# Optimization experiments

Measured on AMD Instinct MI355X. Metric: run time of the kernel, lower is better.

The kernel has to match this reference:

```python
import jax, jax.numpy as jnp
import numpy as np

N_NODES = 50000
N_EDGES = 800000
F_IN = 64
HID = 64
N_GRAPHS = 256
BN_EPS = 1e-5


def setup_inputs() -> dict:
    key = jax.random.key(0)
    ks = jax.random.split(key, 16)
    inp = {
        'x': jax.random.normal(ks[0], (N_NODES, F_IN), dtype=jnp.float32),
        'edge_index': jax.random.randint(ks[1], (2, N_EDGES), 0, N_NODES, dtype=jnp.int64),
        'edge_weight': jax.random.uniform(ks[2], (N_EDGES,), dtype=jnp.float32),
        'batch': jnp.sort(jax.random.randint(ks[3], (N_NODES,), 0, N_GRAPHS, dtype=jnp.int64)),
    }
    def lin(k, fi, fo):
        s = 1.0 / np.sqrt(fi)
        kw, kb = jax.random.split(k)
        return (jax.random.uniform(kw, (fi, fo), jnp.float32, -s, s),
                jax.random.uniform(kb, (fo,), jnp.float32, -s, s))
    inp['W1'], inp['b1'] = lin(ks[4], F_IN, HID)
    inp['W2'], inp['b2'] = lin(ks[5], HID, HID)
    inp['W3'], inp['b3'] = lin(ks[6], HID, HID)
    inp['fcW1'], inp['fcb1'] = lin(ks[7], HID, HID)
    inp['fcW2'], inp['fcb2'] = lin(ks[8], HID, 1)
    for i, k in zip((1, 2, 3), ks[9:12]):
        inp[f'g{i}'] = jnp.ones((HID,), jnp.float32)
        inp[f'be{i}'] = jnp.zeros((HID,), jnp.float32)
    return inp


def gin_conv(x, src, dst, edge_weight, W, b):
    # weighted scatter-add aggregation: agg[dst] += w_e * x[src]
    msg = x[src] * edge_weight[:, None]            # [E, d]
    agg = jax.ops.segment_sum(msg, dst, num_segments=x.shape[0])  # [N, d]
    return (x + agg) @ W + b                       # GIN eps=0, nn = Linear


def batch_norm(x, gamma, beta):
    mu = jnp.mean(x, axis=0)
    var = jnp.var(x, axis=0)
    return (x - mu) * jax.lax.rsqrt(var + BN_EPS) * gamma + beta


def reference(x, edge_index, edge_weight, batch,
              W1, b1, W2, b2, W3, b3, fcW1, fcb1, fcW2, fcb2,
              g1, be1, g2, be2, g3, be3):
    src, dst = edge_index[0], edge_index[1]
    h = batch_norm(jax.nn.relu(gin_conv(x, src, dst, edge_weight, W1, b1)), g1, be1)
    h = batch_norm(jax.nn.relu(gin_conv(h, src, dst, edge_weight, W2, b2)), g2, be2)
    h = batch_norm(gin_conv(h, src, dst, edge_weight, W3, b3), g3, be3)
    pooled = jax.ops.segment_sum(h, batch, num_segments=N_GRAPHS)  # global_add_pool
    h = jax.nn.relu(pooled)
    h = jax.nn.relu(h @ fcW1 + fcb1)
    # dropout is identity in eval / deterministic reference
    return (h @ fcW2 + fcb2).reshape(-1)
```

## Files before the change

kernel.cpp:

```cpp
#include <hip/hip_runtime.h>
#include <hip/hip_bf16.h>


#define NN 50000
#define NE 800000
#define FD 64
#define NG 256
#define CAP 64
#define NBKT 16
#define BN_EPS 1e-5f

#define NPART 8
#define PSIZE 6250
#define ECHUNK 2048
#define NCHUNK ((NE + ECHUNK - 1) / ECHUNK)
#define NBUILD (NCHUNK * NPART)
#define NCVT   ((NN * 16) / 256)

__device__ __forceinline__ float4 dec4(uint2 a) {
    float4 f;
    f.x = __uint_as_float(a.x << 16);
    f.y = __uint_as_float(a.x & 0xFFFF0000u);
    f.z = __uint_as_float(a.y << 16);
    f.w = __uint_as_float(a.y & 0xFFFF0000u);
    return f;
}
__device__ __forceinline__ unsigned rbf(float f) {
    unsigned u = __float_as_uint(f);
    return (u + 0x7FFFu + ((u >> 16) & 1u)) >> 16;
}
__device__ __forceinline__ uint2 enc4(float4 v) {
    uint2 o;
    o.x = rbf(v.x) | (rbf(v.y) << 16);
    o.y = rbf(v.z) | (rbf(v.w) << 16);
    return o;
}

__global__ __launch_bounds__(256) void build_cvt_kernel(
    const int* __restrict__ src, const int* __restrict__ dst,
    const float* __restrict__ ew, int* __restrict__ cursor,
    unsigned* __restrict__ slots,
    const float4* __restrict__ xin, uint2* __restrict__ xout)
{
    int bid = blockIdx.x;
    int tid = threadIdx.x;
    if (bid < NBUILD) {
        int part  = bid & 7;
        int chunk = bid >> 3;
        int base  = chunk * ECHUNK;
        #pragma unroll
        for (int i = 0; i < ECHUNK; i += 256) {
            int e = base + i + tid;
            if (e < NE) {
                int d = dst[e];
                if (d / PSIZE == part) {
                    int pos = atomicAdd(&cursor[d], 1) & (CAP - 1);
                    slots[(size_t)d * CAP + pos] =
                        ((unsigned)src[e] << 16) | rbf(ew[e]);
                }
            }
        }
    } else {
        int i = (bid - NBUILD) * 256 + tid;
        xout[i] = enc4(xin[i]);
    }
}

__global__ __launch_bounds__(256) void agg_layer_kernel(
    const uint2* __restrict__ h, const int* __restrict__ deg,
    const unsigned* __restrict__ slots,
    const float* __restrict__ prev_buckets,
    const float* __restrict__ prev_gamma, const float* __restrict__ prev_beta,
    const float* __restrict__ W, const float* __restrict__ b,
    uint2* __restrict__ y, float* __restrict__ buckets, int relu_flag,
    const int* __restrict__ batch, float* __restrict__ pooled)
{
    __shared__ float Ws[FD * FD];
    __shared__ float ps1[4][FD];
    __shared__ float ps2[4][FD];
    __shared__ float afs[FD], cfs[FD];
    int tid  = threadIdx.x;
    int wave = tid >> 6, lane = tid & 63;
    int g = lane >> 4, l = lane & 15;
    int node = blockIdx.x * 4 + wave;

    {
        float4* Wv = (float4*)Ws;
        const float4* Wg = (const float4*)W;
        #pragma unroll
        for (int i = 0; i < 4; i++) Wv[tid + 256 * i] = Wg[tid + 256 * i];
    }

    unsigned ms = slots[(size_t)node * CAP + lane];
    int dg = deg[node];
    float4 self = dec4(h[(size_t)node * 16 + l]);
    if (dg > CAP) dg = CAP;

    if (prev_buckets) {
        int f = tid & 63, q = tid >> 6;
        float S1 = 0.f, S2 = 0.f;
        #pragma unroll
        for (int i = 0; i < 4; i++) {
            int bkt = q * 4 + i;
            S1 += prev_buckets[bkt * 128 + f];
            S2 += prev_buckets[bkt * 128 + FD + f];
        }
        ps1[q][f] = S1;
        ps2[q][f] = S2;
    }
    __syncthreads();
    if (prev_buckets && tid < FD) {
        float s1 = ps1[0][tid] + ps1[1][tid] + ps1[2][tid] + ps1[3][tid];
        float s2 = ps2[0][tid] + ps2[1][tid] + ps2[2][tid] + ps2[3][tid];
        float mu  = s1 * (1.f / NN);
        float var = s2 * (1.f / NN) - mu * mu;
        float a = prev_gamma[tid] * rsqrtf(var + BN_EPS);
        afs[tid] = a;
        cfs[tid] = prev_beta[tid] - mu * a;
    }
    __syncthreads();

    float4 af = make_float4(1.f, 1.f, 1.f, 1.f);
    float4 cf = make_float4(0.f, 0.f, 0.f, 0.f);
    if (prev_buckets) {
        af = ((const float4*)afs)[l];
        cf = ((const float4*)cfs)[l];
    }

    float4 acc = make_float4(0.f, 0.f, 0.f, 0.f);
    float wsum = 0.f;
    int nIter = (dg + 15) >> 4;
    for (int i = 0; i < nIter; i++) {
        unsigned m[4]; uint2 r[4];
        #pragma unroll
        for (int j = 0; j < 4; j++)
            m[j] = (unsigned)__shfl((int)ms, 16 * i + 4 * j + g, 64);
        #pragma unroll
        for (int j = 0; j < 4; j++)
            r[j] = h[(size_t)(m[j] >> 16) * 16 + l];
        #pragma unroll
        for (int j = 0; j < 4; j++) {
            float w = __uint_as_float(m[j] << 16);
            float4 v = dec4(r[j]);
            wsum += w;
            acc.x = fmaf(w, v.x, acc.x); acc.y = fmaf(w, v.y, acc.y);
            acc.z = fmaf(w, v.z, acc.z); acc.w = fmaf(w, v.w, acc.w);
        }
    }
    acc.x += __shfl_xor(acc.x, 16, 64); acc.y += __shfl_xor(acc.y, 16, 64);
    acc.z += __shfl_xor(acc.z, 16, 64); acc.w += __shfl_xor(acc.w, 16, 64);
    wsum  += __shfl_xor(wsum, 16, 64);
    acc.x += __shfl_xor(acc.x, 32, 64); acc.y += __shfl_xor(acc.y, 32, 64);
    acc.z += __shfl_xor(acc.z, 32, 64); acc.w += __shfl_xor(acc.w, 32, 64);
    wsum  += __shfl_xor(wsum, 32, 64);

    float4 raw;
    raw.x = self.x + acc.x; raw.y = self.y + acc.y;
    raw.z = self.z + acc.z; raw.w = self.w + acc.w;

    float sw = 1.0f + wsum;
    float4 hin;
    hin.x = fmaf(af.x, raw.x, cf.x * sw);
    hin.y = fmaf(af.y, raw.y, cf.y * sw);
    hin.z = fmaf(af.z, raw.z, cf.z * sw);
    hin.w = fmaf(af.w, raw.w, cf.w * sw);

    const float4* __restrict__ WsV = (const float4*)Ws;
    float4 yp = make_float4(0.f, 0.f, 0.f, 0.f);
    #pragma unroll
    for (int kk = 0; kk < 4; kk++) {
        int srcl = 4 * g + kk;
        float a0 = __shfl(hin.x, srcl, 64);
        float a1 = __shfl(hin.y, srcl, 64);
        float a2 = __shfl(hin.z, srcl, 64);
        float a3 = __shfl(hin.w, srcl, 64);
        int k0 = 16 * g + 4 * kk;
        float4 w0 = WsV[(k0 + 0) * 16 + l];
        float4 w1 = WsV[(k0 + 1) * 16 + l];
        float4 w2 = WsV[(k0 + 2) * 16 + l];
        float4 w3 = WsV[(k0 + 3) * 16 + l];
        yp.x = fmaf(a0, w0.x, yp.x); yp.y = fmaf(a0, w0.y, yp.y);
        yp.z = fmaf(a0, w0.z, yp.z); yp.w = fmaf(a0, w0.w, yp.w);
        yp.x = fmaf(a1, w1.x, yp.x); yp.y = fmaf(a1, w1.y, yp.y);
        yp.z = fmaf(a1, w1.z, yp.z); yp.w = fmaf(a1, w1.w, yp.w);
        yp.x = fmaf(a2, w2.x, yp.x); yp.y = fmaf(a2, w2.y, yp.y);
        yp.z = fmaf(a2, w2.z, yp.z); yp.w = fmaf(a2, w2.w, yp.w);
        yp.x = fmaf(a3, w3.x, yp.x); yp.y = fmaf(a3, w3.y, yp.y);
        yp.z = fmaf(a3, w3.z, yp.z); yp.w = fmaf(a3, w3.w, yp.w);
    }
    yp.x += __shfl_xor(yp.x, 16, 64); yp.y += __shfl_xor(yp.y, 16, 64);
    yp.z += __shfl_xor(yp.z, 16, 64); yp.w += __shfl_xor(yp.w, 16, 64);
    yp.x += __shfl_xor(yp.x, 32, 64); yp.y += __shfl_xor(yp.y, 32, 64);
    yp.z += __shfl_xor(yp.z, 32, 64); yp.w += __shfl_xor(yp.w, 32, 64);

    float4 bias = ((const float4*)b)[l];
    float4 yv;
    yv.x = yp.x + bias.x; yv.y = yp.y + bias.y;
    yv.z = yp.z + bias.z; yv.w = yp.w + bias.w;
    if (relu_flag) {
        yv.x = fmaxf(yv.x, 0.f); yv.y = fmaxf(yv.y, 0.f);
        yv.z = fmaxf(yv.z, 0.f); yv.w = fmaxf(yv.w, 0.f);
    }
    if (g == 0) {
        if (!pooled)
            y[(size_t)node * 16 + l] = enc4(yv);
        ((float4*)&ps1[wave][0])[l] = yv;
        float4 sq;
        sq.x = yv.x * yv.x; sq.y = yv.y * yv.y;
        sq.z = yv.z * yv.z; sq.w = yv.w * yv.w;
        ((float4*)&ps2[wave][0])[l] = sq;
    }
    __syncthreads();
    if (tid < FD) {
        float a = ps1[0][tid] + ps1[1][tid] + ps1[2][tid] + ps1[3][tid];
        float q = ps2[0][tid] + ps2[1][tid] + ps2[2][tid] + ps2[3][tid];
        float* bk = buckets + (blockIdx.x & (NBKT - 1)) * 128;
        atomicAdd(&bk[tid], a);
        atomicAdd(&bk[FD + tid], q);
        if (pooled) {
            int n0 = blockIdx.x * 4;
            int b0 = batch[n0], b3 = batch[n0 + 3];
            if (b0 == b3) {
                atomicAdd(&pooled[b0 * FD + tid], a);
            } else {
                #pragma unroll
                for (int w = 0; w < 4; w++)
                    atomicAdd(&pooled[batch[n0 + w] * FD + tid],
                              ps1[w][tid]);
            }
        }
    }
}

__global__ __launch_bounds__(256) void head_kernel(
    const float* __restrict__ pooled, const int* __restrict__ batch,
    const float* __restrict__ buckets3,
    const float* __restrict__ g3, const float* __restrict__ be3,
    const float* __restrict__ fcW1, const float* __restrict__ fcb1,
    const float* __restrict__ fcW2, const float* __restrict__ fcb2,
    float* __restrict__ out)
{
    __shared__ float red[8][FD];
    __shared__ int bounds[2];
    int tid = threadIdx.x;
    int g = blockIdx.x;

    {
        int f = tid & 63, q = tid >> 6;
        float S1 = 0.f, S2 = 0.f;
        #pragma unroll
        for (int i = 0; i < 4; i++) {
            int bkt = q * 4 + i;
            S1 += buckets3[bkt * 128 + f];
            S2 += buckets3[bkt * 128 + FD + f];
        }
        red[q][f]     = S1;
        red[4 + q][f] = S2;
    }
    if (tid < 2) {
        int target = g + tid;
        int lo = 0, hi = NN;
        while (lo < hi) {
            int mid = (lo + hi) >> 1;
            if (batch[mid] < target) lo = mid + 1; else hi = mid;
        }
        bounds[tid] = lo;
    }
    __syncthreads();

    if (tid < 64) {
        float s1 = red[0][tid] + red[1][tid] + red[2][tid] + red[3][tid];
        float s2 = red[4][tid] + red[5][tid] + red[6][tid] + red[7][tid];
        float mu  = s1 * (1.f / NN);
        float var = s2 * (1.f / NN) - mu * mu;
        float a = g3[tid] * rsqrtf(var + BN_EPS);
        float c = be3[tid] - mu * a;

        float cnt = (float)(bounds[1] - bounds[0]);
        float p = pooled[g * FD + tid];
        p = fmaf(a, p, c * cnt);
        p = fmaxf(p, 0.f);
        float acc1 = fcb1[tid];
        #pragma unroll
        for (int k = 0; k < FD; k++) {
            float pk = __shfl(p, k, 64);
            acc1 = fmaf(pk, fcW1[k * FD + tid], acc1);
        }
        acc1 = fmaxf(acc1, 0.f);
        float prod = acc1 * fcW2[tid];
        #pragma unroll
        for (int off = 32; off > 0; off >>= 1)
            prod += __shfl_xor(prod, off, 64);
        if (tid == 0) out[g] = prod + fcb2[0];
    }
}

extern "C" void kernel_launch(void* const* d_in, const int* in_sizes, int n_in,
                              void* d_out, int out_size, void* d_ws, size_t ws_size,
                              hipStream_t stream) {
    const float* x     = (const float*)d_in[0];
    const int*   ei    = (const int*)d_in[1];
    const float* ew    = (const float*)d_in[2];
    const int*   batch = (const int*)d_in[3];
    const float* W1 = (const float*)d_in[4],  *b1 = (const float*)d_in[5];
    const float* W2 = (const float*)d_in[6],  *b2 = (const float*)d_in[7];
    const float* W3 = (const float*)d_in[8],  *b3 = (const float*)d_in[9];
    const float* fcW1 = (const float*)d_in[10], *fcb1 = (const float*)d_in[11];
    const float* fcW2 = (const float*)d_in[12], *fcb2 = (const float*)d_in[13];
    const float* g1 = (const float*)d_in[14], *be1 = (const float*)d_in[15];
    const float* g2 = (const float*)d_in[16], *be2 = (const float*)d_in[17];
    const float* g3 = (const float*)d_in[18], *be3 = (const float*)d_in[19];
    float* out = (float*)d_out;

    const int* srcp = ei;
    const int* dstp = ei + NE;

    char* ws = (char*)d_ws;
    size_t off = 0;
    auto take = [&](size_t bytes) -> char* {
        char* p = ws + off;
        off += (bytes + 255) & ~(size_t)255;
        return p;
    };
    uint2*    xbf   = (uint2*)   take((size_t)NN * FD * 2);
    uint2*    bufA  = (uint2*)   take((size_t)NN * FD * 2);
    uint2*    bufB  = (uint2*)   take((size_t)NN * FD * 2);
    size_t zero_base = off;
    unsigned* slots = (unsigned*)take((size_t)NN * CAP * 4);
    int*      cursor= (int*)     take((size_t)NN * 4);
    float*    buckets=(float*)   take((size_t)3 * NBKT * 128 * 4);
    float*    pooled =(float*)   take((size_t)NG * FD * 4);
    size_t zero_bytes = off - zero_base;
    (void)ws_size; (void)n_in; (void)in_sizes; (void)out_size;

    hipMemsetAsync(ws + zero_base, 0, zero_bytes, stream);

    build_cvt_kernel<<<NBUILD + NCVT, 256, 0, stream>>>(srcp, dstp, ew,
                                                        cursor, slots,
                                                        (const float4*)x, xbf);

    const int gridA = NN / 4;

    float* bk1 = buckets + 0 * NBKT * 128;
    float* bk2 = buckets + 1 * NBKT * 128;
    float* bk3 = buckets + 2 * NBKT * 128;

    agg_layer_kernel<<<gridA, 256, 0, stream>>>(xbf, cursor, slots,
                                                nullptr, nullptr, nullptr,
                                                W1, b1, bufA, bk1, 1,
                                                nullptr, nullptr);
    agg_layer_kernel<<<gridA, 256, 0, stream>>>(bufA, cursor, slots,
                                                bk1, g1, be1,
                                                W2, b2, bufB, bk2, 1,
                                                nullptr, nullptr);
    agg_layer_kernel<<<gridA, 256, 0, stream>>>(bufB, cursor, slots,
                                                bk2, g2, be2,
                                                W3, b3, bufA, bk3, 0,
                                                batch, pooled);
    head_kernel<<<NG, 256, 0, stream>>>(pooled, batch, bk3, g3, be3,
                                        fcW1, fcb1, fcW2, fcb2, out);
}
```

Measured before the change: 261.3 us.

## Hoist BN affine into tiny kernel, template layer modes, defer W smem store

The per-block reduction of the previous layer's BN statistics buckets, along with its two block barriers, moves out of the 12500-block aggregation kernel into a single 64-thread kernel that writes the scale and shift vectors. The aggregation kernel becomes a template on layer mode, so the relu, output-store and pooling branches resolve at compile time. The weight matrix is now loaded into registers at kernel start and only written to shared memory after the gather loop, so the global load overlaps the gather and one barrier remains. In exchange it adds two extra kernel launches and holds more registers across the gather loop, which may lower occupancy.

```diff
diff --git a/kernel.cpp b/kernel.cpp
--- a/kernel.cpp
+++ b/kernel.cpp
@@ -66,65 +66,57 @@
     }
 }
 
+__global__ __launch_bounds__(64) void bn_affine_kernel(
+    const float* __restrict__ bk,
+    const float* __restrict__ gamma, const float* __restrict__ beta,
+    float* __restrict__ afc)
+{
+    int t = threadIdx.x;
+    float S1 = 0.f, S2 = 0.f;
+    #pragma unroll
+    for (int i = 0; i < NBKT; i++) {
+        S1 += bk[i * 128 + t];
+        S2 += bk[i * 128 + FD + t];
+    }
+    float mu  = S1 * (1.f / NN);
+    float var = S2 * (1.f / NN) - mu * mu;
+    float a = gamma[t] * rsqrtf(var + BN_EPS);
+    afc[t]      = a;
+    afc[FD + t] = beta[t] - mu * a;
+}
+
+template<int MODE>
 __global__ __launch_bounds__(256) void agg_layer_kernel(
     const uint2* __restrict__ h, const int* __restrict__ deg,
     const unsigned* __restrict__ slots,
-    const float* __restrict__ prev_buckets,
-    const float* __restrict__ prev_gamma, const float* __restrict__ prev_beta,
+    const float* __restrict__ afc,
     const float* __restrict__ W, const float* __restrict__ b,
-    uint2* __restrict__ y, float* __restrict__ buckets, int relu_flag,
+    uint2* __restrict__ y, float* __restrict__ buckets,
     const int* __restrict__ batch, float* __restrict__ pooled)
 {
     __shared__ float Ws[FD * FD];
     __shared__ float ps1[4][FD];
     __shared__ float ps2[4][FD];
-    __shared__ float afs[FD], cfs[FD];
     int tid  = threadIdx.x;
     int wave = tid >> 6, lane = tid & 63;
     int g = lane >> 4, l = lane & 15;
     int node = blockIdx.x * 4 + wave;
 
-    {
-        float4* Wv = (float4*)Ws;
-        const float4* Wg = (const float4*)W;
-        #pragma unroll
-        for (int i = 0; i < 4; i++) Wv[tid + 256 * i] = Wg[tid + 256 * i];
-    }
+    const float4* __restrict__ Wg = (const float4*)W;
+    float4 wr0 = Wg[tid];
+    float4 wr1 = Wg[tid + 256];
+    float4 wr2 = Wg[tid + 512];
+    float4 wr3 = Wg[tid + 768];
 
     unsigned ms = slots[(size_t)node * CAP + lane];
     int dg = deg[node];
     float4 self = dec4(h[(size_t)node * 16 + l]);
     if (dg > CAP) dg = CAP;
 
-    if (prev_buckets) {
-        int f = tid & 63, q = tid >> 6;
-        float S1 = 0.f, S2 = 0.f;
-        #pragma unroll
-        for (int i = 0; i < 4; i++) {
-            int bkt = q * 4 + i;
-            S1 += prev_buckets[bkt * 128 + f];
-            S2 += prev_buckets[bkt * 128 + FD + f];
-        }
-        ps1[q][f] = S1;
-        ps2[q][f] = S2;
-    }
-    __syncthreads();
-    if (prev_buckets && tid < FD) {
-        float s1 = ps1[0][tid] + ps1[1][tid] + ps1[2][tid] + ps1[3][tid];
-        float s2 = ps2[0][tid] + ps2[1][tid] + ps2[2][tid] + ps2[3][tid];
-        float mu  = s1 * (1.f / NN);
-        float var = s2 * (1.f / NN) - mu * mu;
-        float a = prev_gamma[tid] * rsqrtf(var + BN_EPS);
-        afs[tid] = a;
-        cfs[tid] = prev_beta[tid] - mu * a;
-    }
-    __syncthreads();
-
-    float4 af = make_float4(1.f, 1.f, 1.f, 1.f);
-    float4 cf = make_float4(0.f, 0.f, 0.f, 0.f);
-    if (prev_buckets) {
-        af = ((const float4*)afs)[l];
-        cf = ((const float4*)cfs)[l];
+    float4 af, cf;
+    if (MODE != 0) {
+        af = ((const float4*)afc)[l];
+        cf = ((const float4*)afc)[16 + l];
     }
 
     float4 acc = make_float4(0.f, 0.f, 0.f, 0.f);
@@ -158,12 +150,25 @@
     raw.x = self.x + acc.x; raw.y = self.y + acc.y;
     raw.z = self.z + acc.z; raw.w = self.w + acc.w;
 
-    float sw = 1.0f + wsum;
     float4 hin;
-    hin.x = fmaf(af.x, raw.x, cf.x * sw);
-    hin.y = fmaf(af.y, raw.y, cf.y * sw);
-    hin.z = fmaf(af.z, raw.z, cf.z * sw);
-    hin.w = fmaf(af.w, raw.w, cf.w * sw);
+    if (MODE != 0) {
+        float sw = 1.0f + wsum;
+        hin.x = fmaf(af.x, raw.x, cf.x * sw);
+        hin.y = fmaf(af.y, raw.y, cf.y * sw);
+        hin.z = fmaf(af.z, raw.z, cf.z * sw);
+        hin.w = fmaf(af.w, raw.w, cf.w * sw);
+    } else {
+        hin = raw;
+    }
+
+    {
+        float4* Wv = (float4*)Ws;
+        Wv[tid]       = wr0;
+        Wv[tid + 256] = wr1;
+        Wv[tid + 512] = wr2;
+        Wv[tid + 768] = wr3;
+    }
+    __syncthreads();
 
     const float4* __restrict__ WsV = (const float4*)Ws;
     float4 yp = make_float4(0.f, 0.f, 0.f, 0.f);
@@ -197,12 +202,12 @@
     float4 yv;
     yv.x = yp.x + bias.x; yv.y = yp.y + bias.y;
     yv.z = yp.z + bias.z; yv.w = yp.w + bias.w;
-    if (relu_flag) {
+    if (MODE < 2) {
         yv.x = fmaxf(yv.x, 0.f); yv.y = fmaxf(yv.y, 0.f);
         yv.z = fmaxf(yv.z, 0.f); yv.w = fmaxf(yv.w, 0.f);
     }
     if (g == 0) {
-        if (!pooled)
+        if (MODE < 2)
             y[(size_t)node * 16 + l] = enc4(yv);
         ((float4*)&ps1[wave][0])[l] = yv;
         float4 sq;
@@ -217,7 +222,7 @@
         float* bk = buckets + (blockIdx.x & (NBKT - 1)) * 128;
         atomicAdd(&bk[tid], a);
         atomicAdd(&bk[FD + tid], q);
-        if (pooled) {
+        if (MODE == 2) {
             int n0 = blockIdx.x * 4;
             int b0 = batch[n0], b3 = batch[n0 + 3];
             if (b0 == b3) {
@@ -325,6 +330,8 @@
     uint2*    xbf   = (uint2*)   take((size_t)NN * FD * 2);
     uint2*    bufA  = (uint2*)   take((size_t)NN * FD * 2);
     uint2*    bufB  = (uint2*)   take((size_t)NN * FD * 2);
+    float*    afc1  = (float*)   take((size_t)128 * 4);
+    float*    afc2  = (float*)   take((size_t)128 * 4);
     size_t zero_base = off;
     unsigned* slots = (unsigned*)take((size_t)NN * CAP * 4);
     int*      cursor= (int*)     take((size_t)NN * 4);
@@ -345,18 +352,20 @@
     float* bk2 = buckets + 1 * NBKT * 128;
     float* bk3 = buckets + 2 * NBKT * 128;
 
-    agg_layer_kernel<<<gridA, 256, 0, stream>>>(xbf, cursor, slots,
-                                                nullptr, nullptr, nullptr,
-                                                W1, b1, bufA, bk1, 1,
-                                                nullptr, nullptr);
-    agg_layer_kernel<<<gridA, 256, 0, stream>>>(bufA, cursor, slots,
-                                                bk1, g1, be1,
-                                                W2, b2, bufB, bk2, 1,
-                                                nullptr, nullptr);
-    agg_layer_kernel<<<gridA, 256, 0, stream>>>(bufB, cursor, slots,
-                                                bk2, g2, be2,
-                                                W3, b3, bufA, bk3, 0,
-                                                batch, pooled);
+    agg_layer_kernel<0><<<gridA, 256, 0, stream>>>(xbf, cursor, slots,
+                                                   nullptr,
+                                                   W1, b1, bufA, bk1,
+                                                   nullptr, nullptr);
+    bn_affine_kernel<<<1, 64, 0, stream>>>(bk1, g1, be1, afc1);
+    agg_layer_kernel<1><<<gridA, 256, 0, stream>>>(bufA, cursor, slots,
+                                                   afc1,
+                                                   W2, b2, bufB, bk2,
+                                                   nullptr, nullptr);
+    bn_affine_kernel<<<1, 64, 0, stream>>>(bk2, g2, be2, afc2);
+    agg_layer_kernel<2><<<gridA, 256, 0, stream>>>(bufB, cursor, slots,
+                                                   afc2,
+                                                   W3, b3, nullptr, bk3,
+                                                   batch, pooled);
     head_kernel<<<NG, 256, 0, stream>>>(pooled, batch, bk3, g3, be3,
                                         fcW1, fcb1, fcW2, fcb2, out);
 }
```

Result: no change. 263.7 us (+0.9%).
